# Kernel tuning notes

Hardware: AMD Instinct MI355X
Metric: run time of the kernel (lower is better)

Reference implementation:

```python
import jax, jax.numpy as jnp
import numpy as np

STEPS = 30
BATCH = 1048576
HIDDEN = 32


def setup_inputs() -> dict:
    key = jax.random.key(0)
    k_s, k_w1, k_b1, k_w2, k_b2 = jax.random.split(key, 5)
    return {
        "S": jax.random.normal(k_s, (BATCH, STEPS), dtype=jnp.float32),
        "W1": jax.random.normal(k_w1, (3, HIDDEN), dtype=jnp.float32) * (1.0 / np.sqrt(3.0)),
        "b1": jax.random.normal(k_b1, (HIDDEN,), dtype=jnp.float32) * 0.01,
        "W2": jax.random.normal(k_w2, (HIDDEN, 1), dtype=jnp.float32) * (1.0 / np.sqrt(HIDDEN)),
        "b2": jax.random.normal(k_b2, (1,), dtype=jnp.float32) * 0.01,
        "a_init": jnp.zeros((1,), dtype=jnp.float32),
    }


def reference(S, W1, b1, W2, b2, a_init):
    B = S.shape[0]
    h0 = jnp.zeros((B, 1), dtype=S.dtype)
    d0 = jnp.broadcast_to(a_init.reshape(1, 1), (B, 1))  # a_init.expand(batch, 1)

    def step(carry, s_t):
        h, d_prev = carry
        x = jnp.concatenate([s_t[:, None], d_prev, h], axis=1)  # (B, 3)
        hidden = jax.nn.relu(x @ W1 + b1)                        # (B, 32)
        d = hidden @ W2 + b2                                     # (B, 1)
        h_new = 0.8 * h + 0.2 * d
        return (h_new, d), d

    # scan over time: S.T has shape (steps, B)
    (_, _), deltas = jax.lax.scan(step, (h0, d0), S.T)
    # deltas: (steps, B, 1) -> (B, steps)
    return jnp.transpose(deltas[:, :, 0], (1, 0))
```

## Files before the change

### kernel.cpp

```cpp
#include <hip/hip_runtime.h>

#define STEPS 30
#define HID 32
#define TPB 256
#define EPB 256
#define LDS_STRIDE (STEPS + 1)

typedef float f32x16 __attribute__((ext_vector_type(16)));
typedef __fp16 h8 __attribute__((ext_vector_type(8)));
typedef unsigned int u32x4 __attribute__((ext_vector_type(4)));

static __device__ __forceinline__ unsigned int pkrtz_u32(float x, float y) {
    return __builtin_bit_cast(unsigned int, __builtin_amdgcn_cvt_pkrtz(x, y));
}

__global__ __launch_bounds__(TPB, 4) void hedge_kernel(
    const float* __restrict__ S,
    const float* __restrict__ W1,
    const float* __restrict__ b1,
    const float* __restrict__ W2,
    const float* __restrict__ b2,
    const float* __restrict__ a_init,
    float* __restrict__ out)
{
    __shared__ float tile[EPB * LDS_STRIDE];
    const int tid  = threadIdx.x;
    const int lane = tid & 63;
    const int wv   = tid >> 6;
    const long long base = (long long)blockIdx.x * (EPB * STEPS);

    const float2* S2 = (const float2*)(S + base);
    #pragma unroll
    for (int k = 0; k < (EPB * STEPS) / (2 * TPB); ++k) {
        int i2 = tid + k * TPB;
        float2 v = S2[i2];
        int row = i2 / 15;
        int col = 2 * (i2 - row * 15);
        float* p = &tile[row * LDS_STRIDE + col];
        p[0] = v.x; p[1] = v.y;
    }

    const int j = lane & 31;
    const float wbf = b1[j];
    const float waf = W1[0 * HID + j];
    const float wcf = W1[1 * HID + j];
    const float wef = W1[2 * HID + j];
    u32x4 av;
    if (lane < 32) {
        av[0] = pkrtz_u32(wbf, waf);
        av[1] = pkrtz_u32(wcf, wef);
        av[2] = 0u; av[3] = 0u;
    } else {
        av[0] = 0u; av[1] = 0u; av[2] = 0u; av[3] = 0u;
    }
    const h8 afrag = __builtin_bit_cast(h8, av);

    const int rbase = 4 * (lane >> 5);
    float w2r[16];
    #pragma unroll
    for (int r = 0; r < 16; ++r)
        w2r[r] = W2[(r & 3) + 8 * (r >> 2) + rbase];

    const float bias2 = b2[0];
    const float d_init = a_init[0];
    float dA = d_init, hA = 0.0f;
    float dB = d_init, hB = 0.0f;
    const f32x16 zero16 = {0.f};
    __syncthreads();

    const int erow = 64 * wv + (lane & 31);
    float* myA = &tile[erow * LDS_STRIDE];
    float* myB = &tile[(erow + 32) * LDS_STRIDE];
    #pragma unroll
    for (int t = 0; t < STEPS; ++t) {
        const float sA = myA[t];
        const float sB = myB[t];

        u32x4 bvA, bvB;
        bvA[0] = pkrtz_u32(1.0f, sA);
        bvA[1] = pkrtz_u32(dA, hA);
        bvA[2] = bvA[0]; bvA[3] = bvA[1];
        bvB[0] = pkrtz_u32(1.0f, sB);
        bvB[1] = pkrtz_u32(dB, hB);
        bvB[2] = bvB[0]; bvB[3] = bvB[1];

        const f32x16 PA = __builtin_amdgcn_mfma_f32_32x32x16_f16(
            afrag, __builtin_bit_cast(h8, bvA), zero16, 0, 0, 0);
        const f32x16 PB = __builtin_amdgcn_mfma_f32_32x32x16_f16(
            afrag, __builtin_bit_cast(h8, bvB), zero16, 0, 0, 0);

        float a0 = 0.f, a1 = 0.f, b0 = 0.f, b1v = 0.f;
        #pragma unroll
        for (int r = 0; r < 16; r += 2) {
            a0  = fmaf(w2r[r + 0], fmaxf(PA[r + 0], 0.f), a0);
            a1  = fmaf(w2r[r + 1], fmaxf(PA[r + 1], 0.f), a1);
            b0  = fmaf(w2r[r + 0], fmaxf(PB[r + 0], 0.f), b0);
            b1v = fmaf(w2r[r + 1], fmaxf(PB[r + 1], 0.f), b1v);
        }
        float partA = a0 + a1;
        float partB = b0 + b1v;
        partA += __shfl_xor(partA, 32);
        partB += __shfl_xor(partB, 32);
        const float dnA = bias2 + partA;
        const float dnB = bias2 + partB;
        hA = fmaf(0.2f, dnA, 0.8f * hA);
        hB = fmaf(0.2f, dnB, 0.8f * hB);
        dA = dnA;
        dB = dnB;
        if (lane < 32) {
            myA[t] = dnA;
            myB[t] = dnB;
        }
    }
    __syncthreads();

    float2* O2 = (float2*)(out + base);
    #pragma unroll
    for (int k = 0; k < (EPB * STEPS) / (2 * TPB); ++k) {
        int i2 = tid + k * TPB;
        int row = i2 / 15;
        int col = 2 * (i2 - row * 15);
        const float* p = &tile[row * LDS_STRIDE + col];
        O2[i2] = make_float2(p[0], p[1]);
    }
}

extern "C" void kernel_launch(void* const* d_in, const int* in_sizes, int n_in,
                              void* d_out, int out_size, void* d_ws, size_t ws_size,
                              hipStream_t stream) {
    const float* S      = (const float*)d_in[0];
    const float* W1     = (const float*)d_in[1];
    const float* b1     = (const float*)d_in[2];
    const float* W2     = (const float*)d_in[3];
    const float* b2     = (const float*)d_in[4];
    const float* a_init = (const float*)d_in[5];
    float* out = (float*)d_out;

    const int batch = in_sizes[0] / STEPS;
    const int grid  = batch / EPB;
    hedge_kernel<<<grid, TPB, 0, stream>>>(S, W1, b1, W2, b2, a_init, out);
}
```

Measured before the change: 252.9 us.

## Compute second layer projection with MFMA instead of VALU FMAs and shuffle

Replaces the per-lane W2 dot product and cross-half shuffle with extra fp16 MFMA ops. The ReLU outputs are packed to half precision as B operands, and W2 is packed into A fragments held only by row-0 lanes, so the reduction across hidden units happens in the matrix unit. This removes the VALU FMAs and the DPP/shuffle from the serial per-step chain. In exchange it adds four MFMAs per step on the critical latency path and rounds the hidden activations to fp16. Launch bounds are also relaxed from 4 to 2 waves-per-EU minimum.

```diff
diff --git a/kernel.cpp b/kernel.cpp
--- a/kernel.cpp
+++ b/kernel.cpp
@@ -14,7 +14,7 @@
     return __builtin_bit_cast(unsigned int, __builtin_amdgcn_cvt_pkrtz(x, y));
 }
 
-__global__ __launch_bounds__(TPB, 4) void hedge_kernel(
+__global__ __launch_bounds__(TPB, 2) void hedge_kernel(
     const float* __restrict__ S,
     const float* __restrict__ W1,
     const float* __restrict__ b1,
@@ -41,25 +41,27 @@
     }
 
     const int j = lane & 31;
-    const float wbf = b1[j];
-    const float waf = W1[0 * HID + j];
-    const float wcf = W1[1 * HID + j];
-    const float wef = W1[2 * HID + j];
-    u32x4 av;
+    u32x4 av = {0u, 0u, 0u, 0u};
     if (lane < 32) {
-        av[0] = pkrtz_u32(wbf, waf);
-        av[1] = pkrtz_u32(wcf, wef);
-        av[2] = 0u; av[3] = 0u;
-    } else {
-        av[0] = 0u; av[1] = 0u; av[2] = 0u; av[3] = 0u;
+        av[0] = pkrtz_u32(b1[j], W1[0 * HID + j]);
+        av[1] = pkrtz_u32(W1[1 * HID + j], W1[2 * HID + j]);
     }
     const h8 afrag = __builtin_bit_cast(h8, av);
 
-    const int rbase = 4 * (lane >> 5);
-    float w2r[16];
-    #pragma unroll
-    for (int r = 0; r < 16; ++r)
-        w2r[r] = W2[(r & 3) + 8 * (r >> 2) + rbase];
+    u32x4 avB1 = {0u, 0u, 0u, 0u}, avB2 = {0u, 0u, 0u, 0u};
+    if ((lane & 31) == 0) {
+        const int rb = 4 * (lane >> 5);
+        avB1[0] = pkrtz_u32(W2[0 + rb],  W2[1 + rb]);
+        avB1[1] = pkrtz_u32(W2[2 + rb],  W2[3 + rb]);
+        avB1[2] = pkrtz_u32(W2[8 + rb],  W2[9 + rb]);
+        avB1[3] = pkrtz_u32(W2[10 + rb], W2[11 + rb]);
+        avB2[0] = pkrtz_u32(W2[16 + rb], W2[17 + rb]);
+        avB2[1] = pkrtz_u32(W2[18 + rb], W2[19 + rb]);
+        avB2[2] = pkrtz_u32(W2[24 + rb], W2[25 + rb]);
+        avB2[3] = pkrtz_u32(W2[26 + rb], W2[27 + rb]);
+    }
+    const h8 afragB1 = __builtin_bit_cast(h8, avB1);
+    const h8 afragB2 = __builtin_bit_cast(h8, avB2);
 
     const float bias2 = b2[0];
     const float d_init = a_init[0];
@@ -89,20 +91,26 @@
         const f32x16 PB = __builtin_amdgcn_mfma_f32_32x32x16_f16(
             afrag, __builtin_bit_cast(h8, bvB), zero16, 0, 0, 0);
 
-        float a0 = 0.f, a1 = 0.f, b0 = 0.f, b1v = 0.f;
+        u32x4 zA1, zA2, zB1, zB2;
         #pragma unroll
-        for (int r = 0; r < 16; r += 2) {
-            a0  = fmaf(w2r[r + 0], fmaxf(PA[r + 0], 0.f), a0);
-            a1  = fmaf(w2r[r + 1], fmaxf(PA[r + 1], 0.f), a1);
-            b0  = fmaf(w2r[r + 0], fmaxf(PB[r + 0], 0.f), b0);
-            b1v = fmaf(w2r[r + 1], fmaxf(PB[r + 1], 0.f), b1v);
+        for (int i = 0; i < 4; ++i) {
+            zA1[i] = pkrtz_u32(fmaxf(PA[2*i + 0], 0.f), fmaxf(PA[2*i + 1], 0.f));
+            zA2[i] = pkrtz_u32(fmaxf(PA[2*i + 8], 0.f), fmaxf(PA[2*i + 9], 0.f));
+            zB1[i] = pkrtz_u32(fmaxf(PB[2*i + 0], 0.f), fmaxf(PB[2*i + 1], 0.f));
+            zB2[i] = pkrtz_u32(fmaxf(PB[2*i + 8], 0.f), fmaxf(PB[2*i + 9], 0.f));
         }
-        float partA = a0 + a1;
-        float partB = b0 + b1v;
-        partA += __shfl_xor(partA, 32);
-        partB += __shfl_xor(partB, 32);
-        const float dnA = bias2 + partA;
-        const float dnB = bias2 + partB;
+
+        const f32x16 yA1 = __builtin_amdgcn_mfma_f32_32x32x16_f16(
+            afragB1, __builtin_bit_cast(h8, zA1), zero16, 0, 0, 0);
+        const f32x16 yA2 = __builtin_amdgcn_mfma_f32_32x32x16_f16(
+            afragB2, __builtin_bit_cast(h8, zA2), zero16, 0, 0, 0);
+        const f32x16 yB1 = __builtin_amdgcn_mfma_f32_32x32x16_f16(
+            afragB1, __builtin_bit_cast(h8, zB1), zero16, 0, 0, 0);
+        const f32x16 yB2 = __builtin_amdgcn_mfma_f32_32x32x16_f16(
+            afragB2, __builtin_bit_cast(h8, zB2), zero16, 0, 0, 0);
+
+        const float dnA = (yA1[0] + yA2[0]) + bias2;
+        const float dnB = (yB1[0] + yB2[0]) + bias2;
         hA = fmaf(0.2f, dnA, 0.8f * hA);
         hB = fmaf(0.2f, dnB, 0.8f * hB);
         dA = dnA;
```

Measured after the change: 264.2 us. 1.04x slower.
